# Optimization experiments

Measured on AMD Instinct MI355X. Metric: run time of the kernel, lower is better.

The kernel has to match this reference:

```python
import jax, jax.numpy as jnp
import numpy as np

B, S, D_IN, D_HEAD = 4, 4096, 1024, 64

def setup_inputs() -> dict:
    key = jax.random.key(0)
    k1, k2, k3, k4 = jax.random.split(key, 4)
    scale = 0.02
    return {
        "input_vectors": jax.random.normal(k1, (B, S, D_IN), dtype=jnp.float32),
        "Wq": jax.random.normal(k2, (D_IN, D_HEAD), dtype=jnp.float32) * scale,
        "Wk": jax.random.normal(k3, (D_IN, D_HEAD), dtype=jnp.float32) * scale,
        "Wv": jax.random.normal(k4, (D_IN, D_HEAD), dtype=jnp.float32) * scale,
    }

def reference(input_vectors, Wq, Wk, Wv):
    # QKV projections (Linear with no bias): [B,S,d_in] @ [d_in,d_head]
    q = input_vectors @ Wq  # [B,S,H]
    k = input_vectors @ Wk
    v = input_vectors @ Wv
    n = input_vectors.shape[1]
    # causal attention scores: [B,S,S]
    scores = jnp.einsum('bqh,bkh->bqk', q, k)
    causal = jnp.tril(jnp.ones((n, n), dtype=bool))  # True = keep
    scores = jnp.where(causal, scores, -jnp.inf)
    scale = k.shape[-1] ** -0.5
    attn = jax.nn.softmax(scores * scale, axis=-1)
    return jnp.einsum('bqk,bkh->bqh', attn, v)
```

## Files before the change

### kernel.cpp

```cpp
#include <hip/hip_runtime.h>
#include <stdint.h>

#define SEQ   4096
#define DIN   1024

typedef __attribute__((ext_vector_type(8))) short bf16x8;
typedef __attribute__((ext_vector_type(4))) float floatx4;
typedef __attribute__((ext_vector_type(4))) unsigned short ushortx4;

#if __has_builtin(__builtin_amdgcn_exp2f)
#define EXP2(x) __builtin_amdgcn_exp2f(x)
#else
#define EXP2(x) exp2f(x)
#endif

__device__ __forceinline__ unsigned short f2bf(float f) {
    union { float f; unsigned int u; } v; v.f = f;
    unsigned int u = v.u + 0x7fffu + ((v.u >> 16) & 1u);
    return (unsigned short)(u >> 16);
}
__device__ __forceinline__ float bf2f(unsigned short h) {
    union { unsigned int u; float f; } v; v.u = ((unsigned int)h) << 16;
    return v.f;
}
__device__ __forceinline__ float uasf(unsigned int u) {
    union { unsigned int u; float f; } v; v.u = u; return v.f;
}
__device__ __forceinline__ unsigned int fasu(float f) {
    union { float f; unsigned int u; } v; v.f = f; return v.u;
}

__global__ void wt_prep(const float* __restrict__ Wq, const float* __restrict__ Wk,
                        const float* __restrict__ Wv, unsigned short* __restrict__ WT) {
    int idx = blockIdx.x * 256 + threadIdx.x;
    int k   = idx & 1023;
    int n   = (idx >> 10) & 63;
    int mat = idx >> 16;
    const float* W = (mat == 0) ? Wq : ((mat == 1) ? Wk : Wv);
    WT[idx] = f2bf(W[k * 64 + n]);
}

#define QSCALE 0.18033688011112042f
__launch_bounds__(512, 2)
__global__ void proj_qkv(const float* __restrict__ X, const unsigned short* __restrict__ WT,
                         unsigned short* __restrict__ qb, unsigned short* __restrict__ kb,
                         unsigned short* __restrict__ vb) {
    __shared__ __align__(16) float          X0[64 * 64], X1[64 * 64];
    __shared__ __align__(16) unsigned short W0[192 * 64], W1[192 * 64];
    const int tid = threadIdx.x;
    const int wave = tid >> 6, lane = tid & 63;
    const int quad = lane >> 4, l16 = lane & 15;
    const int strip = wave >> 1;
    const int cg = wave & 1;
    const int row0 = blockIdx.x * 64;
    const int m = strip * 16 + l16;

    floatx4 acc[6];
#pragma unroll
    for (int i = 0; i < 6; i++) acc[i] = (floatx4){0.f, 0.f, 0.f, 0.f};

    int xu[2], xr[2], xc[2], wu[3], wr[3], wc[3];
#pragma unroll
    for (int i = 0; i < 2; i++) {
        xu[i] = i * 512 + tid; xr[i] = xu[i] >> 4; xc[i] = (xu[i] & 15) ^ (xr[i] & 15);
    }
#pragma unroll
    for (int i = 0; i < 3; i++) {
        wu[i] = i * 512 + tid; wr[i] = wu[i] >> 3; wc[i] = (wu[i] & 7) ^ (wr[i] & 7);
    }
    floatx4 xpre[2], wpre[3];
    auto issue = [&](int k0) {
#pragma unroll
        for (int i = 0; i < 2; i++)
            xpre[i] = *(const floatx4*)(X + (size_t)(row0 + xr[i]) * DIN + k0 + xc[i] * 4);
#pragma unroll
        for (int i = 0; i < 3; i++)
            wpre[i] = *(const floatx4*)(WT + (size_t)wr[i] * 1024 + k0 + wc[i] * 8);
    };

    issue(0);
    for (int kc = 0; kc < 16; kc++) {
        float*          Xd = (kc & 1) ? X1 : X0;
        unsigned short* Wd = (kc & 1) ? W1 : W0;
#pragma unroll
        for (int i = 0; i < 2; i++) *(floatx4*)&Xd[xu[i] * 4] = xpre[i];
#pragma unroll
        for (int i = 0; i < 3; i++) *(floatx4*)&Wd[wu[i] * 8] = wpre[i];
        if (kc < 15) issue((kc + 1) * 64);
        __syncthreads();

        bf16x8 af[2];
#pragma unroll
        for (int ks = 0; ks < 2; ks++) {
            floatx4 x0 = *(const floatx4*)&Xd[m * 64 + ((ks * 8 + quad * 2 + 0) ^ (m & 15)) * 4];
            floatx4 x1 = *(const floatx4*)&Xd[m * 64 + ((ks * 8 + quad * 2 + 1) ^ (m & 15)) * 4];
#pragma unroll
            for (int j = 0; j < 4; j++) {
                af[ks][j]     = (short)f2bf(x0[j]);
                af[ks][j + 4] = (short)f2bf(x1[j]);
            }
        }
#pragma unroll
        for (int i = 0; i < 6; i++) {
            const int nrow = (cg * 6 + i) * 16 + l16;
#pragma unroll
            for (int ks = 0; ks < 2; ks++) {
                const int c = ks * 4 + quad;
                bf16x8 bfrag = *(const bf16x8*)&Wd[nrow * 64 + (c ^ (nrow & 7)) * 8];
                acc[i] = __builtin_amdgcn_mfma_f32_16x16x32_bf16(af[ks], bfrag, acc[i], 0, 0, 0);
            }
        }
    }
#pragma unroll
    for (int i = 0; i < 6; i++) {
        const int nt = cg * 6 + i;
        const int mat = nt >> 2;
        const int col = (nt & 3) * 16 + l16;
#pragma unroll
        for (int r = 0; r < 4; r++) {
            const int orow = row0 + strip * 16 + quad * 4 + r;
            float v = acc[i][r];
            if (mat == 0) {
                qb[(size_t)orow * 64 + col] = f2bf(v * QSCALE);
            } else if (mat == 1) {
                kb[(size_t)orow * 64 + col] = f2bf(v);
            } else {
                int b = orow >> 12, sq = orow & 4095;
                vb[((size_t)b * 64 + col) * SEQ + sq] = f2bf(v);
            }
        }
    }
}

__launch_bounds__(256, 4)
__global__ void attn(const unsigned short* __restrict__ qb, const unsigned short* __restrict__ kb,
                     const unsigned short* __restrict__ vb, unsigned short* __restrict__ opart,
                     float* __restrict__ lpart) {
    __shared__ __align__(16) unsigned short Kl[64 * 64];
    __shared__ __align__(16) unsigned short Vl[64 * 64];
    __shared__ __align__(16) unsigned short Pl[4][16 * 72];

    const int bid = blockIdx.x;
    const int qt = 63 - (bid >> 4);
    const int batch = (bid >> 2) & 3;
    const int s = bid & 3;
    const int q0 = qt * 64;
    const int T = qt + 1;
    const int lo = (T * s) >> 2, hi = (T * (s + 1)) >> 2;

    const int tid = threadIdx.x;
    const int wave = tid >> 6, lane = tid & 63;
    const int quad = lane >> 4, l16 = lane & 15;

    const unsigned short* qr = qb + (size_t)(batch * SEQ + q0 + wave * 16 + l16) * 64;
    bf16x8 qa0 = *(const bf16x8*)(qr + quad * 8);
    bf16x8 qa1 = *(const bf16x8*)(qr + 32 + quad * 8);

    floatx4 o[4];
#pragma unroll
    for (int i = 0; i < 4; i++) o[i] = (floatx4){0.f, 0.f, 0.f, 0.f};
    float lsum = 0.f;

    const unsigned short* kbase = kb + (size_t)batch * SEQ * 64;
    const unsigned short* vbase = vb + (size_t)batch * 64 * SEQ;
    unsigned short* P = &Pl[wave][0];

    int ku[2], kr[2], kc_[2], vu[2], vd[2], vc[2];
#pragma unroll
    for (int i = 0; i < 2; i++) {
        ku[i] = i * 256 + tid; kr[i] = ku[i] >> 3; kc_[i] = (ku[i] & 7) ^ (kr[i] & 7);
        vu[i] = i * 256 + tid; vd[i] = vu[i] >> 3; vc[i] = (vu[i] & 7) ^ (vd[i] & 7);
    }
    floatx4 kpre[2], vpre[2];
    auto issue = [&](int k0) {
#pragma unroll
        for (int i = 0; i < 2; i++)
            kpre[i] = *(const floatx4*)(kbase + (size_t)(k0 + kr[i]) * 64 + kc_[i] * 8);
#pragma unroll
        for (int i = 0; i < 2; i++)
            vpre[i] = *(const floatx4*)(vbase + (size_t)vd[i] * SEQ + k0 + vc[i] * 8);
    };

    if (lo < hi) issue(lo * 64);
    for (int kt = lo; kt < hi; kt++) {
        __syncthreads();
#pragma unroll
        for (int i = 0; i < 2; i++) *(floatx4*)&Kl[ku[i] * 8] = kpre[i];
#pragma unroll
        for (int i = 0; i < 2; i++) *(floatx4*)&Vl[vu[i] * 8] = vpre[i];
        if (kt + 1 < hi) issue((kt + 1) * 64);
        __syncthreads();

        const int k0 = kt * 64;
        floatx4 sc[4];
#pragma unroll
        for (int nt = 0; nt < 4; nt++) {
            sc[nt] = (floatx4){0.f, 0.f, 0.f, 0.f};
            const int key = nt * 16 + l16;
#pragma unroll
            for (int ks = 0; ks < 2; ks++) {
                const int c = ks * 4 + quad;
                bf16x8 ak = *(const bf16x8*)&Kl[key * 64 + (c ^ (key & 7)) * 8];
                sc[nt] = __builtin_amdgcn_mfma_f32_16x16x32_bf16(
                    ak, ks == 0 ? qa0 : qa1, sc[nt], 0, 0, 0);
            }
        }
        if (kt == T - 1) {
            const int qg = q0 + wave * 16 + l16;
#pragma unroll
            for (int nt = 0; nt < 4; nt++) {
#pragma unroll
                for (int r = 0; r < 4; r++) {
                    const int kg = k0 + nt * 16 + quad * 4 + r;
                    if (kg > qg) sc[nt][r] = -1e30f;
                }
            }
        }
#pragma unroll
        for (int nt = 0; nt < 4; nt++) {
            float v0 = EXP2(sc[nt][0]), v1 = EXP2(sc[nt][1]);
            float v2 = EXP2(sc[nt][2]), v3 = EXP2(sc[nt][3]);
            unsigned int u0 = fasu(v0) & 0xffff0000u, u1 = fasu(v1) & 0xffff0000u;
            unsigned int u2 = fasu(v2) & 0xffff0000u, u3 = fasu(v3) & 0xffff0000u;
            lsum += (uasf(u0) + uasf(u1)) + (uasf(u2) + uasf(u3));
            uint2 w;
            w.x = (u0 >> 16) | u1;
            w.y = (u2 >> 16) | u3;
            *(uint2*)&P[l16 * 72 + nt * 16 + quad * 4] = w;
        }
#pragma unroll
        for (int ks = 0; ks < 2; ks++) {
            bf16x8 pb = *(const bf16x8*)&P[l16 * 72 + ks * 32 + quad * 8];
#pragma unroll
            for (int nt = 0; nt < 4; nt++) {
                const int d = nt * 16 + l16;
                bf16x8 av = *(const bf16x8*)&Vl[d * 64 + ((ks * 4 + quad) ^ (d & 7)) * 8];
                o[nt] = __builtin_amdgcn_mfma_f32_16x16x32_bf16(av, pb, o[nt], 0, 0, 0);
            }
        }
    }

    unsigned short* ob = opart + (size_t)s * (4 * SEQ * 64)
                       + (size_t)(batch * SEQ + q0 + wave * 16) * 64;
    float* lb = lpart + (size_t)s * (4 * SEQ) + (batch * SEQ + q0 + wave * 16);
    float l = lsum;
    l += __shfl_xor(l, 16);
    l += __shfl_xor(l, 32);
#pragma unroll
    for (int nt = 0; nt < 4; nt++) {
        ushortx4 w;
#pragma unroll
        for (int r = 0; r < 4; r++) w[r] = f2bf(o[nt][r]);
        *(ushortx4*)&ob[l16 * 64 + nt * 16 + quad * 4] = w;
    }
    if (quad == 0) lb[l16] = l;
}

__global__ void merge(const unsigned short* __restrict__ opart, const float* __restrict__ lpart,
                      float* __restrict__ out) {
    int idx = blockIdx.x * 256 + threadIdx.x;
    int row = idx >> 4, c4 = idx & 15;
    float l = lpart[row] + lpart[4 * SEQ + row] + lpart[8 * SEQ + row] + lpart[12 * SEQ + row];
    float inv = 1.f / l;
    floatx4 acc = (floatx4){0.f, 0.f, 0.f, 0.f};
#pragma unroll
    for (int s = 0; s < 4; s++) {
        ushortx4 u = *(const ushortx4*)(opart + (size_t)s * (4 * SEQ * 64)
                                        + (size_t)row * 64 + c4 * 4);
#pragma unroll
        for (int j = 0; j < 4; j++) acc[j] += bf2f(u[j]);
    }
    acc *= inv;
    *(floatx4*)(out + (size_t)row * 64 + c4 * 4) = acc;
}

extern "C" void kernel_launch(void* const* d_in, const int* in_sizes, int n_in,
                              void* d_out, int out_size, void* d_ws, size_t ws_size,
                              hipStream_t stream) {
    const float* X  = (const float*)d_in[0];
    const float* Wq = (const float*)d_in[1];
    const float* Wk = (const float*)d_in[2];
    const float* Wv = (const float*)d_in[3];
    float* out = (float*)d_out;
    char* ws = (char*)d_ws;
    unsigned short* WT    = (unsigned short*)(ws + 0);
    unsigned short* qb    = (unsigned short*)(ws + 393216);
    unsigned short* kb    = (unsigned short*)(ws + 2490368);
    unsigned short* vb    = (unsigned short*)(ws + 4587520);
    unsigned short* opart = (unsigned short*)(ws + 6684672);
    float*          lpart = (float*)(ws + 15073280);

    hipLaunchKernelGGL(wt_prep,  dim3(768),  dim3(256), 0, stream, Wq, Wk, Wv, WT);
    hipLaunchKernelGGL(proj_qkv, dim3(256),  dim3(512), 0, stream, X, WT, qb, kb, vb);
    hipLaunchKernelGGL(attn,     dim3(1024), dim3(256), 0, stream, qb, kb, vb, opart, lpart);
    hipLaunchKernelGGL(merge,    dim3(1024), dim3(256), 0, stream, opart, lpart, out);
}
```

Measured before the change: 135.1 us.

## Use 128-row query tiles, double-buffer K/V, split keys 8 ways, coalesce weight transpose

```diff
diff --git a/kernel.cpp b/kernel.cpp
--- a/kernel.cpp
+++ b/kernel.cpp
@@ -32,12 +32,26 @@
 
 __global__ void wt_prep(const float* __restrict__ Wq, const float* __restrict__ Wk,
                         const float* __restrict__ Wv, unsigned short* __restrict__ WT) {
-    int idx = blockIdx.x * 256 + threadIdx.x;
-    int k   = idx & 1023;
-    int n   = (idx >> 10) & 63;
-    int mat = idx >> 16;
+    __shared__ float Tt[64][65];
+    const int tid = threadIdx.x;
+    const int mat = blockIdx.x >> 4, kt = blockIdx.x & 15, k0 = kt * 64;
     const float* W = (mat == 0) ? Wq : ((mat == 1) ? Wk : Wv);
-    WT[idx] = f2bf(W[k * 64 + n]);
+#pragma unroll
+    for (int i = 0; i < 4; i++) {
+        int u = i * 256 + tid, r = u >> 4, c = u & 15;
+        floatx4 ld = *(const floatx4*)(W + (size_t)(k0 + r) * 64 + c * 4);
+#pragma unroll
+        for (int j = 0; j < 4; j++) Tt[r][c * 4 + j] = ld[j];
+    }
+    __syncthreads();
+#pragma unroll
+    for (int i = 0; i < 2; i++) {
+        int v = i * 256 + tid, n = v >> 3, k8 = v & 7;
+        bf16x8 w;
+#pragma unroll
+        for (int j = 0; j < 8; j++) w[j] = (short)f2bf(Tt[k8 * 8 + j][n]);
+        *(bf16x8*)&WT[(size_t)(mat * 64 + n) * 1024 + k0 + k8 * 8] = w;
+    }
 }
 
 #define QSCALE 0.18033688011112042f
@@ -132,34 +146,39 @@
     }
 }
 
-__launch_bounds__(256, 4)
+__launch_bounds__(256, 3)
 __global__ void attn(const unsigned short* __restrict__ qb, const unsigned short* __restrict__ kb,
                      const unsigned short* __restrict__ vb, unsigned short* __restrict__ opart,
                      float* __restrict__ lpart) {
-    __shared__ __align__(16) unsigned short Kl[64 * 64];
-    __shared__ __align__(16) unsigned short Vl[64 * 64];
-    __shared__ __align__(16) unsigned short Pl[4][16 * 72];
+    __shared__ __align__(16) unsigned short K0[64 * 64], K1[64 * 64];
+    __shared__ __align__(16) unsigned short V0[64 * 64], V1[64 * 64];
+    __shared__ __align__(16) unsigned short Pl[4][32 * 72];
 
     const int bid = blockIdx.x;
-    const int qt = 63 - (bid >> 4);
-    const int batch = (bid >> 2) & 3;
-    const int s = bid & 3;
-    const int q0 = qt * 64;
-    const int T = qt + 1;
-    const int lo = (T * s) >> 2, hi = (T * (s + 1)) >> 2;
+    const int qt = 31 - (bid >> 5);
+    const int batch = (bid >> 3) & 3;
+    const int s = bid & 7;
+    const int q0 = qt * 128;
+    const int T = 2 * qt + 2;
+    const int lo = (T * s) >> 3, hi = (T * (s + 1)) >> 3;
 
     const int tid = threadIdx.x;
     const int wave = tid >> 6, lane = tid & 63;
     const int quad = lane >> 4, l16 = lane & 15;
 
-    const unsigned short* qr = qb + (size_t)(batch * SEQ + q0 + wave * 16 + l16) * 64;
-    bf16x8 qa0 = *(const bf16x8*)(qr + quad * 8);
-    bf16x8 qa1 = *(const bf16x8*)(qr + 32 + quad * 8);
-
-    floatx4 o[4];
-#pragma unroll
-    for (int i = 0; i < 4; i++) o[i] = (floatx4){0.f, 0.f, 0.f, 0.f};
-    float lsum = 0.f;
+    const unsigned short* qr = qb + (size_t)(batch * SEQ + q0 + wave * 32 + l16) * 64;
+    bf16x8 qa[2][2];
+    qa[0][0] = *(const bf16x8*)(qr + quad * 8);
+    qa[0][1] = *(const bf16x8*)(qr + 32 + quad * 8);
+    qa[1][0] = *(const bf16x8*)(qr + 16 * 64 + quad * 8);
+    qa[1][1] = *(const bf16x8*)(qr + 16 * 64 + 32 + quad * 8);
+
+    floatx4 o[2][4];
+#pragma unroll
+    for (int st = 0; st < 2; st++)
+#pragma unroll
+        for (int i = 0; i < 4; i++) o[st][i] = (floatx4){0.f, 0.f, 0.f, 0.f};
+    float ls[2] = {0.f, 0.f};
 
     const unsigned short* kbase = kb + (size_t)batch * SEQ * 64;
     const unsigned short* vbase = vb + (size_t)batch * 64 * SEQ;
@@ -183,88 +202,103 @@
 
     if (lo < hi) issue(lo * 64);
     for (int kt = lo; kt < hi; kt++) {
-        __syncthreads();
-#pragma unroll
-        for (int i = 0; i < 2; i++) *(floatx4*)&Kl[ku[i] * 8] = kpre[i];
-#pragma unroll
-        for (int i = 0; i < 2; i++) *(floatx4*)&Vl[vu[i] * 8] = vpre[i];
+        unsigned short* Kd = (kt & 1) ? K1 : K0;
+        unsigned short* Vd = (kt & 1) ? V1 : V0;
+#pragma unroll
+        for (int i = 0; i < 2; i++) *(floatx4*)&Kd[ku[i] * 8] = kpre[i];
+#pragma unroll
+        for (int i = 0; i < 2; i++) *(floatx4*)&Vd[vu[i] * 8] = vpre[i];
         if (kt + 1 < hi) issue((kt + 1) * 64);
         __syncthreads();
 
         const int k0 = kt * 64;
-        floatx4 sc[4];
-#pragma unroll
-        for (int nt = 0; nt < 4; nt++) {
-            sc[nt] = (floatx4){0.f, 0.f, 0.f, 0.f};
-            const int key = nt * 16 + l16;
-#pragma unroll
-            for (int ks = 0; ks < 2; ks++) {
-                const int c = ks * 4 + quad;
-                bf16x8 ak = *(const bf16x8*)&Kl[key * 64 + (c ^ (key & 7)) * 8];
-                sc[nt] = __builtin_amdgcn_mfma_f32_16x16x32_bf16(
-                    ak, ks == 0 ? qa0 : qa1, sc[nt], 0, 0, 0);
-            }
-        }
-        if (kt == T - 1) {
-            const int qg = q0 + wave * 16 + l16;
+        floatx4 sc[2][4];
+#pragma unroll
+        for (int st = 0; st < 2; st++)
+#pragma unroll
+            for (int nt = 0; nt < 4; nt++) sc[st][nt] = (floatx4){0.f, 0.f, 0.f, 0.f};
+#pragma unroll
+        for (int ks = 0; ks < 2; ks++) {
 #pragma unroll
             for (int nt = 0; nt < 4; nt++) {
-#pragma unroll
-                for (int r = 0; r < 4; r++) {
-                    const int kg = k0 + nt * 16 + quad * 4 + r;
-                    if (kg > qg) sc[nt][r] = -1e30f;
-                }
-            }
-        }
-#pragma unroll
-        for (int nt = 0; nt < 4; nt++) {
-            float v0 = EXP2(sc[nt][0]), v1 = EXP2(sc[nt][1]);
-            float v2 = EXP2(sc[nt][2]), v3 = EXP2(sc[nt][3]);
-            unsigned int u0 = fasu(v0) & 0xffff0000u, u1 = fasu(v1) & 0xffff0000u;
-            unsigned int u2 = fasu(v2) & 0xffff0000u, u3 = fasu(v3) & 0xffff0000u;
-            lsum += (uasf(u0) + uasf(u1)) + (uasf(u2) + uasf(u3));
-            uint2 w;
-            w.x = (u0 >> 16) | u1;
-            w.y = (u2 >> 16) | u3;
-            *(uint2*)&P[l16 * 72 + nt * 16 + quad * 4] = w;
+                const int key = nt * 16 + l16;
+                bf16x8 ak = *(const bf16x8*)&Kd[key * 64 + (((ks * 4 + quad)) ^ (key & 7)) * 8];
+                sc[0][nt] = __builtin_amdgcn_mfma_f32_16x16x32_bf16(ak, qa[0][ks], sc[0][nt], 0, 0, 0);
+                sc[1][nt] = __builtin_amdgcn_mfma_f32_16x16x32_bf16(ak, qa[1][ks], sc[1][nt], 0, 0, 0);
+            }
+        }
+        if (kt >= T - 2) {
+#pragma unroll
+            for (int st = 0; st < 2; st++) {
+                const int qg = q0 + wave * 32 + st * 16 + l16;
+#pragma unroll
+                for (int nt = 0; nt < 4; nt++)
+#pragma unroll
+                    for (int r = 0; r < 4; r++) {
+                        const int kg = k0 + nt * 16 + quad * 4 + r;
+                        if (kg > qg) sc[st][nt][r] = -1e30f;
+                    }
+            }
+        }
+#pragma unroll
+        for (int st = 0; st < 2; st++) {
+#pragma unroll
+            for (int nt = 0; nt < 4; nt++) {
+                float v0 = EXP2(sc[st][nt][0]), v1 = EXP2(sc[st][nt][1]);
+                float v2 = EXP2(sc[st][nt][2]), v3 = EXP2(sc[st][nt][3]);
+                unsigned int u0 = fasu(v0) & 0xffff0000u, u1 = fasu(v1) & 0xffff0000u;
+                unsigned int u2 = fasu(v2) & 0xffff0000u, u3 = fasu(v3) & 0xffff0000u;
+                ls[st] += (uasf(u0) + uasf(u1)) + (uasf(u2) + uasf(u3));
+                uint2 w;
+                w.x = (u0 >> 16) | u1;
+                w.y = (u2 >> 16) | u3;
+                *(uint2*)&P[(st * 16 + l16) * 72 + nt * 16 + quad * 4] = w;
+            }
         }
 #pragma unroll
         for (int ks = 0; ks < 2; ks++) {
-            bf16x8 pb = *(const bf16x8*)&P[l16 * 72 + ks * 32 + quad * 8];
+            bf16x8 pb0 = *(const bf16x8*)&P[(0  + l16) * 72 + ks * 32 + quad * 8];
+            bf16x8 pb1 = *(const bf16x8*)&P[(16 + l16) * 72 + ks * 32 + quad * 8];
 #pragma unroll
             for (int nt = 0; nt < 4; nt++) {
                 const int d = nt * 16 + l16;
-                bf16x8 av = *(const bf16x8*)&Vl[d * 64 + ((ks * 4 + quad) ^ (d & 7)) * 8];
-                o[nt] = __builtin_amdgcn_mfma_f32_16x16x32_bf16(av, pb, o[nt], 0, 0, 0);
+                bf16x8 av = *(const bf16x8*)&Vd[d * 64 + (((ks * 4 + quad)) ^ (d & 7)) * 8];
+                o[0][nt] = __builtin_amdgcn_mfma_f32_16x16x32_bf16(av, pb0, o[0][nt], 0, 0, 0);
+                o[1][nt] = __builtin_amdgcn_mfma_f32_16x16x32_bf16(av, pb1, o[1][nt], 0, 0, 0);
             }
         }
     }
 
     unsigned short* ob = opart + (size_t)s * (4 * SEQ * 64)
-                       + (size_t)(batch * SEQ + q0 + wave * 16) * 64;
-    float* lb = lpart + (size_t)s * (4 * SEQ) + (batch * SEQ + q0 + wave * 16);
-    float l = lsum;
-    l += __shfl_xor(l, 16);
-    l += __shfl_xor(l, 32);
-#pragma unroll
-    for (int nt = 0; nt < 4; nt++) {
-        ushortx4 w;
-#pragma unroll
-        for (int r = 0; r < 4; r++) w[r] = f2bf(o[nt][r]);
-        *(ushortx4*)&ob[l16 * 64 + nt * 16 + quad * 4] = w;
-    }
-    if (quad == 0) lb[l16] = l;
+                       + (size_t)(batch * SEQ + q0 + wave * 32) * 64;
+    float* lb = lpart + (size_t)s * (4 * SEQ) + (batch * SEQ + q0 + wave * 32);
+#pragma unroll
+    for (int st = 0; st < 2; st++) {
+        float l = ls[st];
+        l += __shfl_xor(l, 16);
+        l += __shfl_xor(l, 32);
+#pragma unroll
+        for (int nt = 0; nt < 4; nt++) {
+            ushortx4 w;
+#pragma unroll
+            for (int r = 0; r < 4; r++) w[r] = f2bf(o[st][nt][r]);
+            *(ushortx4*)&ob[(st * 16 + l16) * 64 + nt * 16 + quad * 4] = w;
+        }
+        if (quad == 0) lb[st * 16 + l16] = l;
+    }
 }
 
 __global__ void merge(const unsigned short* __restrict__ opart, const float* __restrict__ lpart,
                       float* __restrict__ out) {
     int idx = blockIdx.x * 256 + threadIdx.x;
     int row = idx >> 4, c4 = idx & 15;
-    float l = lpart[row] + lpart[4 * SEQ + row] + lpart[8 * SEQ + row] + lpart[12 * SEQ + row];
+    float l = 0.f;
+#pragma unroll
+    for (int s = 0; s < 8; s++) l += lpart[s * 4 * SEQ + row];
     float inv = 1.f / l;
     floatx4 acc = (floatx4){0.f, 0.f, 0.f, 0.f};
 #pragma unroll
-    for (int s = 0; s < 4; s++) {
+    for (int s = 0; s < 8; s++) {
         ushortx4 u = *(const ushortx4*)(opart + (size_t)s * (4 * SEQ * 64)
                                         + (size_t)row * 64 + c4 * 4);
 #pragma unroll
@@ -288,9 +322,9 @@
     unsigned short* kb    = (unsigned short*)(ws + 2490368);
     unsigned short* vb    = (unsigned short*)(ws + 4587520);
     unsigned short* opart = (unsigned short*)(ws + 6684672);
-    float*          lpart = (float*)(ws + 15073280);
-
-    hipLaunchKernelGGL(wt_prep,  dim3(768),  dim3(256), 0, stream, Wq, Wk, Wv, WT);
+    float*          lpart = (float*)(ws + 23461888);
+
+    hipLaunchKernelGGL(wt_prep,  dim3(48),   dim3(256), 0, stream, Wq, Wk, Wv, WT);
     hipLaunchKernelGGL(proj_qkv, dim3(256),  dim3(512), 0, stream, X, WT, qb, kb, vb);
     hipLaunchKernelGGL(attn,     dim3(1024), dim3(256), 0, stream, qb, kb, vb, opart, lpart);
     hipLaunchKernelGGL(merge,    dim3(1024), dim3(256), 0, stream, opart, lpart, out);
```

Result: no change. 135.5 us (+0.3%).
